# Kernel tuning notes

Hardware: AMD Instinct MI355X
Metric: run time of the kernel (lower is better)

The kernel has to match this reference:

```python
import jax, jax.numpy as jnp
import numpy as np

WS = 8
HEADS = 8


def _conv3(x, w, groups=1):
    return jax.lax.conv_general_dilated(
        x, w, (1, 1), 'SAME',
        dimension_numbers=('NCHW', 'OIHW', 'NCHW'),
        feature_group_count=groups)


def _bn(x, g, b, eps=1e-5):
    # training-mode batchnorm (batch statistics), per-channel over (B,H,W)
    m = x.mean(axis=(0, 2, 3), keepdims=True)
    v = x.var(axis=(0, 2, 3), keepdims=True)
    return (x - m) * jax.lax.rsqrt(v + eps) * g[None, :, None, None] + b[None, :, None, None]


def _relu6(x):
    return jnp.clip(x, 0.0, 6.0)


def _forward(x, w_iem, g_iem, b_iem, w_nem, g_nem, b_nem,
             w_iem_dw, w_nem_dw, w_q, w_k, w_v, w_proj, temperature):
    b, C, hp, wp = x.shape
    heads = temperature.shape[1]
    d = C // heads
    ws = WS
    nh, nw = hp // ws, wp // ws  # H,W chosen divisible by ws -> no padding

    iem_out = _relu6(_bn(_conv3(x, w_iem), g_iem, b_iem))
    illumination_map = _conv3(iem_out, w_iem_dw, groups=C)
    nem_out = _relu6(_bn(_conv3(x, w_nem), g_nem, b_nem))
    noise_map = _conv3(nem_out, w_nem_dw, groups=C)

    illum_scalar = illumination_map.mean(axis=1, keepdims=True)  # [b,1,H,W]
    noise_scalar = noise_map.mean(axis=1, keepdims=True)

    # 1x1 convs as channel matmuls
    q = jnp.einsum('oc,bchw->bohw', w_q, illumination_map)
    k = jnp.einsum('oc,bchw->bohw', w_k, noise_map)
    v = jnp.einsum('oc,bchw->bohw', w_v, x)

    def to_windows(t):  # [b,C,H,W] -> [b,heads,nh,nw,ws*ws,d]
        t = t.reshape(b, heads, d, hp, wp).transpose(0, 1, 3, 4, 2)
        t = t.reshape(b, heads, nh, ws, nw, ws, d).transpose(0, 1, 2, 4, 3, 5, 6)
        return t.reshape(b, heads, nh, nw, ws * ws, d)

    def scalar_to_windows(t):  # [b,1,H,W] -> [b,1,nh,nw,ws*ws,1]
        t = t.reshape(b, 1, nh, ws, nw, ws).transpose(0, 1, 2, 4, 3, 5)
        return t.reshape(b, 1, nh, nw, ws * ws, 1)

    qw, kw, vw = to_windows(q), to_windows(k), to_windows(v)
    illum_w = scalar_to_windows(illum_scalar)
    noise_w = scalar_to_windows(noise_scalar)

    qw = qw / jnp.maximum(jnp.linalg.norm(qw, axis=-1, keepdims=True), 1e-12)
    kw = kw / jnp.maximum(jnp.linalg.norm(kw, axis=-1, keepdims=True), 1e-12)
    qw = qw * (1.0 + illum_w)
    kw = kw * jnp.clip(1.0 - noise_w, 0.0, 1.0)

    scale = d ** (-0.5)
    attn = jnp.einsum('bhnmqd,bhnmkd->bhnmqk', qw, kw) * scale
    attn = attn * temperature  # temperature: [1,heads,1,1,1,1]
    attn = jax.nn.softmax(attn, axis=-1)
    outw = jnp.einsum('bhnmqk,bhnmkd->bhnmqd', attn, vw)

    outw = outw.reshape(b, heads, nh, nw, ws, ws, d).transpose(0, 1, 6, 2, 4, 3, 5)
    out = outw.reshape(b, C, hp, wp)
    return jnp.einsum('oc,bchw->bohw', w_proj, out)


def setup_inputs() -> dict:
    key = jax.random.key(0)
    ks = jax.random.split(key, 10)
    C = 256
    B, H, W = 2, 256, 256

    def w(k, shape):
        return jax.random.normal(k, shape, jnp.float32) * 0.05

    return {
        'x': jax.random.normal(ks[0], (B, C, H, W), jnp.float32),
        'w_iem': w(ks[1], (C, C, 3, 3)),
        'g_iem': jnp.ones((C,), jnp.float32),
        'b_iem': jnp.zeros((C,), jnp.float32),
        'w_nem': w(ks[2], (C, C, 3, 3)),
        'g_nem': jnp.ones((C,), jnp.float32),
        'b_nem': jnp.zeros((C,), jnp.float32),
        'w_iem_dw': w(ks[3], (C, 1, 3, 3)),
        'w_nem_dw': w(ks[4], (C, 1, 3, 3)),
        'w_q': w(ks[5], (C, C)),
        'w_k': w(ks[6], (C, C)),
        'w_v': w(ks[7], (C, C)),
        'w_proj': w(ks[8], (C, C)),
        'temperature': jnp.ones((1, HEADS, 1, 1, 1, 1), jnp.float32),
    }


def reference(x, w_iem, g_iem, b_iem, w_nem, g_nem, b_nem,
              w_iem_dw, w_nem_dw, w_q, w_k, w_v, w_proj, temperature):
    return _forward(x, w_iem, g_iem, b_iem, w_nem, g_nem, b_nem,
                    w_iem_dw, w_nem_dw, w_q, w_k, w_v, w_proj, temperature)
```

## Files before the change

kernel.cpp:

```cpp
#include <hip/hip_runtime.h>
#include <math.h>

constexpr int Bn  = 2;
constexpr int C   = 256;
constexpr int H   = 256;
constexpr int W   = 256;
constexpr int HW  = H * W;
constexpr size_t CHW = (size_t)C * HW;

typedef __bf16 bf16x8 __attribute__((ext_vector_type(8)));
typedef float  f32x4  __attribute__((ext_vector_type(4)));

__device__ __forceinline__ unsigned short f2bf(float f) {
    unsigned int u = __float_as_uint(f);
    u += 0x7fffu + ((u >> 16) & 1u);
    return (unsigned short)(u >> 16);
}
__device__ __forceinline__ float bf2f(unsigned short h) {
    return __uint_as_float(((unsigned int)h) << 16);
}
__device__ __forceinline__ float bflo(unsigned int u) { return __uint_as_float(u << 16); }
__device__ __forceinline__ float bfhi(unsigned int u) { return __uint_as_float(u & 0xffff0000u); }

__device__ __forceinline__ bf16x8 u2b(uint4 u) {
    union { uint4 a; bf16x8 b; } c; c.a = u; return c.b;
}

__device__ __forceinline__ void gld_lds16(const void* g, void* lds) {
    __builtin_amdgcn_global_load_lds(
        (const __attribute__((address_space(1))) unsigned int*)g,
        (__attribute__((address_space(3))) unsigned int*)lds, 16, 0, 0);
}

__device__ __forceinline__ int swz2048(int bid) {
    return ((bid & 7) << 8) | (bid >> 3);
}

__global__ __launch_bounds__(256) void packx_k(
    const float* __restrict__ x, unsigned short* __restrict__ xT)
{
    __shared__ float tl[64][65];
    const int id = blockIdx.x;
    const int ct = id & 3;
    const size_t px0 = (size_t)(id >> 2) * 64;
    const int b  = (int)(px0 >> 16);
    const int hw = (int)(px0 & 65535);
    const int c0 = ct * 64;
    const int t  = threadIdx.x;

    {
        const int cl = t >> 2, pseg = t & 3;
        const float* src = x + ((size_t)(b * C + c0 + cl)) * HW + hw + pseg * 16;
#pragma unroll
        for (int i = 0; i < 4; i++) {
            float4 v = *(const float4*)(src + i * 4);
            tl[cl][pseg * 16 + i * 4 + 0] = v.x;
            tl[cl][pseg * 16 + i * 4 + 1] = v.y;
            tl[cl][pseg * 16 + i * 4 + 2] = v.z;
            tl[cl][pseg * 16 + i * 4 + 3] = v.w;
        }
    }
    __syncthreads();
    {
        const int pl = t >> 2, csec = t & 3;
        __attribute__((aligned(16))) unsigned short rv[16];
#pragma unroll
        for (int j = 0; j < 16; j++) rv[j] = f2bf(tl[csec * 16 + j][pl]);
        unsigned short* dst = xT + (px0 + pl) * C + c0 + csec * 16;
        *(uint4*)dst       = *(const uint4*)&rv[0];
        *(uint4*)(dst + 8) = *(const uint4*)&rv[8];
    }
}

__global__ __launch_bounds__(256) void pack_k(
    const float* __restrict__ w, unsigned short* __restrict__ out, int taps)
{
    const int e = blockIdx.x * 256 + threadIdx.x;
    const int kslot = e & 31;
    const int ocl   = (e >> 5) & 127;
    const int icc   = (e >> 12) & 7;
    const int oct   = (e >> 15) & 1;
    const int off   = e >> 16;
    const int oc = oct * 128 + ocl;
    const int q  = kslot >> 3, j = kslot & 7;
    const int ic = icc * 32 + ((q ^ ((ocl >> 2) & 3)) << 3) + j;
    out[e] = f2bf(w[((size_t)oc * C + ic) * taps + off]);
}

__global__ __launch_bounds__(256) void pack4_k(
    const float* __restrict__ wq, const float* __restrict__ wk,
    const float* __restrict__ wv, const float* __restrict__ wp,
    unsigned short* __restrict__ oq, unsigned short* __restrict__ ok,
    unsigned short* __restrict__ ov, unsigned short* __restrict__ op)
{
    const int bid  = blockIdx.x;
    const int wsel = bid >> 8;
    const int e    = (bid & 255) * 256 + threadIdx.x;
    const float* w = (wsel == 0) ? wq : (wsel == 1) ? wk : (wsel == 2) ? wv : wp;
    unsigned short* out = (wsel == 0) ? oq : (wsel == 1) ? ok : (wsel == 2) ? ov : op;
    const int kslot = e & 31;
    const int ocl   = (e >> 5) & 127;
    const int icc   = (e >> 12) & 7;
    const int oct   = (e >> 15) & 1;
    const int oc = oct * 128 + ocl;
    const int q  = kslot >> 3, j = kslot & 7;
    const int ic = icc * 32 + ((q ^ ((ocl >> 2) & 3)) << 3) + j;
    out[e] = f2bf(w[(size_t)oc * C + ic]);
}

__global__ __launch_bounds__(256, 2) void conv2_k(
    const unsigned short* __restrict__ xT,
    const unsigned short* __restrict__ Wp0, const unsigned short* __restrict__ Wp1,
    unsigned short* __restrict__ out0, unsigned short* __restrict__ out1,
    const unsigned short* __restrict__ zbuf, float* __restrict__ stats_part)
{
    __shared__ unsigned short As[2][2][128 * 32];
    __shared__ unsigned short Bs[2][128 * 32];
    __shared__ float sstat[2][128][2];

    const int id  = swz2048(blockIdx.x);
    const int oct = id & 1;
    const int ch  = (id >> 1) & 1;
    const int r   = (id >> 2) & 255;
    const int b   = id >> 10;
    const int px0 = ch * 128;

    const int t  = threadIdx.x;
    const int wv = t >> 6;
    const int l  = t & 63;
    const int wm = (wv >> 1) * 64;
    const int wn = (wv & 1) * 64;

    ((float*)sstat)[t]       = 0.f;
    ((float*)sstat)[t + 256] = 0.f;

    const int qp = (l >> 4) ^ ((l >> 2) & 3);
    int a_off[4], b_off[4];
#pragma unroll
    for (int i = 0; i < 4; i++) {
        a_off[i] = (wm + i * 16 + (l & 15)) * 64 + qp * 16;
        b_off[i] = (wn + i * 16 + (l & 15)) * 64 + qp * 16;
    }
    const int spx_base = wv * 32 + (l >> 2);
    const int skk0 = (((l & 3) ^ (l >> 4)) << 3);

    const int off_lo = (r == 0) ? 3 : 0;
    const int off_hi = (r == 255) ? 6 : 9;

    f32x4 acc[2][4][4];
#pragma unroll
    for (int s = 0; s < 2; s++)
#pragma unroll
        for (int i = 0; i < 4; i++)
#pragma unroll
            for (int j = 0; j < 4; j++) acc[s][i][j] = (f32x4){0.f, 0.f, 0.f, 0.f};

#pragma unroll 1
    for (int off = off_lo; off < off_hi; ++off) {
        const int dy = off / 3, dx = off - dy * 3;
        const int rr = r + dy - 1;
        const size_t rowpix = (size_t)(b * HW) + (size_t)rr * W;
#pragma unroll 1
        for (int ip = 0; ip < 4; ++ip) {
            __syncthreads();
            const size_t wofs = ((size_t)(((off * 2 + oct) * 8 + ip * 2)) * 4096) * 2
                                + wv * 2048 + l * 16;
#pragma unroll
            for (int kc = 0; kc < 2; kc++) {
                char* A0 = (char*)As[0][kc] + wv * 2048;
                char* A1 = (char*)As[1][kc] + wv * 2048;
                const size_t o = wofs + (size_t)kc * 8192;
                gld_lds16((const char*)Wp0 + o, A0);
                gld_lds16((const char*)Wp0 + o + 1024, A0 + 1024);
                gld_lds16((const char*)Wp1 + o, A1);
                gld_lds16((const char*)Wp1 + o + 1024, A1 + 1024);
                const int ic0 = (ip * 2 + kc) * 32;
                char* BsB = (char*)Bs[kc] + wv * 2048;
#pragma unroll
                for (int i = 0; i < 2; i++) {
                    const int px = spx_base + i * 16;
                    const int cx = px0 + px + dx - 1;
                    const void* g = ((unsigned)cx > 255u)
                        ? (const void*)zbuf
                        : (const void*)(xT + ((rowpix + cx) * C + ic0 + skk0));
                    gld_lds16(g, BsB + i * 1024);
                }
            }
            asm volatile("s_waitcnt vmcnt(0)" ::: "memory");
            __syncthreads();
#pragma unroll
            for (int kc = 0; kc < 2; kc++) {
                bf16x8 af0[4], af1[4], bfr[4];
#pragma unroll
                for (int i = 0; i < 4; i++) {
                    af0[i] = *(const bf16x8*)((const char*)As[0][kc] + a_off[i]);
                    af1[i] = *(const bf16x8*)((const char*)As[1][kc] + a_off[i]);
                }
#pragma unroll
                for (int i = 0; i < 4; i++)
                    bfr[i] = *(const bf16x8*)((const char*)Bs[kc] + b_off[i]);
#pragma unroll
                for (int mi = 0; mi < 4; mi++)
#pragma unroll
                    for (int nj = 0; nj < 4; nj++) {
                        acc[0][mi][nj] = __builtin_amdgcn_mfma_f32_16x16x32_bf16(
                            af0[mi], bfr[nj], acc[0][mi][nj], 0, 0, 0);
                        acc[1][mi][nj] = __builtin_amdgcn_mfma_f32_16x16x32_bf16(
                            af1[mi], bfr[nj], acc[1][mi][nj], 0, 0, 0);
                    }
            }
        }
    }

    const int colpx = px0 + wn + (l & 15);
    const int rowoc = oct * 128 + wm + (l >> 4) * 4;
#pragma unroll
    for (int s = 0; s < 2; s++) {
        unsigned short* ob = s ? out1 : out0;
#pragma unroll
        for (int mi = 0; mi < 4; mi++) {
#pragma unroll
            for (int rg = 0; rg < 4; rg++) {
                const int oc = rowoc + mi * 16 + rg;
                float ps = 0.f, pq = 0.f;
#pragma unroll
                for (int nj = 0; nj < 4; nj++) {
                    const float v = acc[s][mi][nj][rg];
                    ps += v;
                    pq = fmaf(v, v, pq);
                    const int px = colpx + nj * 16;
                    const size_t idx = ((size_t)(b * C + oc)) * HW + (size_t)r * W + px;
                    ob[idx] = f2bf(v);
                }
                ps += __shfl_xor(ps, 1);  pq += __shfl_xor(pq, 1);
                ps += __shfl_xor(ps, 2);  pq += __shfl_xor(pq, 2);
                ps += __shfl_xor(ps, 4);  pq += __shfl_xor(pq, 4);
                ps += __shfl_xor(ps, 8);  pq += __shfl_xor(pq, 8);
                if ((l & 15) == 0) {
                    const int loc = wm + (l >> 4) * 4 + mi * 16 + rg;
                    atomicAdd(&sstat[s][loc][0], ps);
                    atomicAdd(&sstat[s][loc][1], pq);
                }
            }
        }
    }
    __syncthreads();
    stats_part[(size_t)id * 512 + t * 2 + 0] = ((float(*)[2])sstat)[t][0];
    stats_part[(size_t)id * 512 + t * 2 + 1] = ((float(*)[2])sstat)[t][1];
}

__global__ __launch_bounds__(256) void bn_reduce_k(
    const float* __restrict__ stats_part,
    const float* __restrict__ g0, const float* __restrict__ b0,
    const float* __restrict__ g1, const float* __restrict__ b1,
    float* __restrict__ scl0, float* __restrict__ shf0,
    float* __restrict__ scl1, float* __restrict__ shf1)
{
    const int s   = blockIdx.x >> 8;
    const int gc  = blockIdx.x & 255;
    const int oct = gc >> 7;
    const int loc = gc & 127;
    const int t   = threadIdx.x;
    const int ent = (s * 128 + loc) * 2;

    float ps = 0.f, pq = 0.f;
#pragma unroll
    for (int m = 0; m < 4; m++) {
        const int id = oct + 2 * (t + 256 * m);
        ps += stats_part[(size_t)id * 512 + ent];
        pq += stats_part[(size_t)id * 512 + ent + 1];
    }
    __shared__ float rs[256], rq[256];
    rs[t] = ps; rq[t] = pq;
    __syncthreads();
    for (int o = 128; o > 0; o >>= 1) {
        if (t < o) { rs[t] += rs[t + o]; rq[t] += rq[t + o]; }
        __syncthreads();
    }
    if (t == 0) {
        const float n    = (float)Bn * HW;
        const float mean = rs[0] / n;
        const float var  = rq[0] / n - mean * mean;
        const float g    = s ? g1[gc] : g0[gc];
        const float be   = s ? b1[gc] : b0[gc];
        const float sc   = g * rsqrtf(var + 1e-5f);
        if (s) { scl1[gc] = sc; shf1[gc] = be - mean * sc; }
        else   { scl0[gc] = sc; shf0[gc] = be - mean * sc; }
    }
}

__global__ __launch_bounds__(256, 2) void gemm2_k(
    const unsigned short* __restrict__ qin, const unsigned short* __restrict__ kin,
    const unsigned short* __restrict__ Wpq, const unsigned short* __restrict__ Wpk,
    unsigned short* __restrict__ outq, unsigned short* __restrict__ outk)
{
    __shared__ unsigned short As[2][2][128 * 32];
    __shared__ unsigned short Bs[2][2][128 * 32];

    const int id  = swz2048(blockIdx.x);
    const int oct = id & 1;
    const int ch  = (id >> 1) & 1;
    const int r   = (id >> 2) & 255;
    const int b   = id >> 10;
    const int px0 = ch * 128;

    const int t  = threadIdx.x;
    const int wv = t >> 6;
    const int l  = t & 63;
    const int wm = (wv >> 1) * 64;
    const int wn = (wv & 1) * 64;

    const int qp = (l >> 4) ^ ((l >> 2) & 3);
    int a_off[4], b_off[4];
#pragma unroll
    for (int i = 0; i < 4; i++) {
        a_off[i] = (wm + i * 16 + (l & 15)) * 64 + qp * 16;
        b_off[i] = (wn + i * 16 + (l & 15)) * 64 + qp * 16;
    }
    const int spx_base = wv * 32 + (l >> 2);
    const int skk0 = (((l & 3) ^ (l >> 4)) << 3);

    const size_t rowpix = (size_t)(b * HW) + (size_t)r * W;

    f32x4 acc[2][4][4];
#pragma unroll
    for (int s = 0; s < 2; s++)
#pragma unroll
        for (int i = 0; i < 4; i++)
#pragma unroll
            for (int j = 0; j < 4; j++) acc[s][i][j] = (f32x4){0.f, 0.f, 0.f, 0.f};

#pragma unroll 1
    for (int ip = 0; ip < 4; ++ip) {
        __syncthreads();
#pragma unroll
        for (int kc = 0; kc < 2; kc++) {
            const int icc = ip * 2 + kc;
            const size_t wofs = ((size_t)(oct * 8 + icc) * 4096) * 2 + wv * 2048 + l * 16;
            char* Aq = (char*)As[0][kc] + wv * 2048;
            char* Ak = (char*)As[1][kc] + wv * 2048;
            gld_lds16((const char*)Wpq + wofs, Aq);
            gld_lds16((const char*)Wpq + wofs + 1024, Aq + 1024);
            gld_lds16((const char*)Wpk + wofs, Ak);
            gld_lds16((const char*)Wpk + wofs + 1024, Ak + 1024);
            const int ic0 = icc * 32;
            char* Bq = (char*)Bs[0][kc] + wv * 2048;
            char* Bk = (char*)Bs[1][kc] + wv * 2048;
#pragma unroll
            for (int i = 0; i < 2; i++) {
                const int cx = px0 + spx_base + i * 16;
                gld_lds16((const void*)(qin + ((rowpix + cx) * C + ic0 + skk0)), Bq + i * 1024);
                gld_lds16((const void*)(kin + ((rowpix + cx) * C + ic0 + skk0)), Bk + i * 1024);
            }
        }
        asm volatile("s_waitcnt vmcnt(0)" ::: "memory");
        __syncthreads();
#pragma unroll
        for (int kc = 0; kc < 2; kc++) {
#pragma unroll
            for (int s = 0; s < 2; s++) {
                bf16x8 af[4], bfr[4];
#pragma unroll
                for (int i = 0; i < 4; i++) {
                    af[i]  = *(const bf16x8*)((const char*)As[s][kc] + a_off[i]);
                    bfr[i] = *(const bf16x8*)((const char*)Bs[s][kc] + b_off[i]);
                }
#pragma unroll
                for (int mi = 0; mi < 4; mi++)
#pragma unroll
                    for (int nj = 0; nj < 4; nj++)
                        acc[s][mi][nj] = __builtin_amdgcn_mfma_f32_16x16x32_bf16(
                            af[mi], bfr[nj], acc[s][mi][nj], 0, 0, 0);
            }
        }
    }

    const int colpx = px0 + wn + (l & 15);
    const int rowoc = oct * 128 + wm + (l >> 4) * 4;
    const size_t pxg = (size_t)(b * HW) + (size_t)r * W;
#pragma unroll
    for (int s = 0; s < 2; s++) {
        unsigned short* ob = s ? outk : outq;
#pragma unroll
        for (int mi = 0; mi < 4; mi++) {
#pragma unroll
            for (int nj = 0; nj < 4; nj++) {
                __attribute__((aligned(8))) unsigned short rv[4];
#pragma unroll
                for (int rg = 0; rg < 4; rg++) rv[rg] = f2bf(acc[s][mi][nj][rg]);
                const int oc = rowoc + mi * 16;
                const int px = colpx + nj * 16;
                *(uint2*)(ob + (pxg + px) * C + oc) = *(const uint2*)rv;
            }
        }
    }
}

template<bool F32OUT, bool NHWC_OUT>
__global__ __launch_bounds__(256, 4) void gemm_k(
    const unsigned short* __restrict__ xT, const unsigned short* __restrict__ Wp,
    unsigned short* __restrict__ outb, float* __restrict__ outf)
{
    __shared__ unsigned short As[2][128 * 32];
    __shared__ unsigned short Bs[2][128 * 32];

    const int id  = swz2048(blockIdx.x);
    const int oct = id & 1;
    const int ch  = (id >> 1) & 1;
    const int r   = (id >> 2) & 255;
    const int b   = id >> 10;
    const int px0 = ch * 128;

    const int t  = threadIdx.x;
    const int wv = t >> 6;
    const int l  = t & 63;
    const int wm = (wv >> 1) * 64;
    const int wn = (wv & 1) * 64;

    const int qp = (l >> 4) ^ ((l >> 2) & 3);
    int a_off[4], b_off[4];
#pragma unroll
    for (int i = 0; i < 4; i++) {
        a_off[i] = (wm + i * 16 + (l & 15)) * 64 + qp * 16;
        b_off[i] = (wn + i * 16 + (l & 15)) * 64 + qp * 16;
    }
    const int spx_base = wv * 32 + (l >> 2);
    const int skk0 = (((l & 3) ^ (l >> 4)) << 3);

    const size_t rowpix = (size_t)(b * HW) + (size_t)r * W;

    f32x4 acc[4][4];
#pragma unroll
    for (int i = 0; i < 4; i++)
#pragma unroll
        for (int j = 0; j < 4; j++) acc[i][j] = (f32x4){0.f, 0.f, 0.f, 0.f};

#pragma unroll 1
    for (int ip = 0; ip < 4; ++ip) {
        __syncthreads();
#pragma unroll
        for (int kc = 0; kc < 2; kc++) {
            const int icc = ip * 2 + kc;
            const char* Ag = (const char*)Wp +
                ((size_t)(oct * 8 + icc) * 4096) * 2 + wv * 2048 + l * 16;
            char* AsB = (char*)As[kc] + wv * 2048;
            gld_lds16(Ag, AsB);
            gld_lds16(Ag + 1024, AsB + 1024);
            const int ic0 = icc * 32;
            char* BsB = (char*)Bs[kc] + wv * 2048;
#pragma unroll
            for (int i = 0; i < 2; i++) {
                const int cx = px0 + spx_base + i * 16;
                gld_lds16((const void*)(xT + ((rowpix + cx) * C + ic0 + skk0)), BsB + i * 1024);
            }
        }
        asm volatile("s_waitcnt vmcnt(0)" ::: "memory");
        __syncthreads();
#pragma unroll
        for (int kc = 0; kc < 2; kc++) {
            bf16x8 af[4], bfr[4];
#pragma unroll
            for (int i = 0; i < 4; i++) {
                af[i]  = *(const bf16x8*)((const char*)As[kc] + a_off[i]);
                bfr[i] = *(const bf16x8*)((const char*)Bs[kc] + b_off[i]);
            }
#pragma unroll
            for (int mi = 0; mi < 4; mi++)
#pragma unroll
                for (int nj = 0; nj < 4; nj++)
                    acc[mi][nj] = __builtin_amdgcn_mfma_f32_16x16x32_bf16(
                        af[mi], bfr[nj], acc[mi][nj], 0, 0, 0);
        }
    }

    const int colpx = px0 + wn + (l & 15);
    const int rowoc = oct * 128 + wm + (l >> 4) * 4;
    if (NHWC_OUT) {
        const size_t pxg = (size_t)(b * HW) + (size_t)r * W;
#pragma unroll
        for (int mi = 0; mi < 4; mi++) {
#pragma unroll
            for (int nj = 0; nj < 4; nj++) {
                __attribute__((aligned(8))) unsigned short rv[4];
#pragma unroll
                for (int rg = 0; rg < 4; rg++) rv[rg] = f2bf(acc[mi][nj][rg]);
                const int oc = rowoc + mi * 16;
                const int px = colpx + nj * 16;
                *(uint2*)(outb + (pxg + px) * C + oc) = *(const uint2*)rv;
            }
        }
    } else {
#pragma unroll
        for (int mi = 0; mi < 4; mi++) {
#pragma unroll
            for (int nj = 0; nj < 4; nj++) {
#pragma unroll
                for (int rg = 0; rg < 4; rg++) {
                    const int oc = rowoc + mi * 16 + rg;
                    const int px = colpx + nj * 16;
                    const size_t idx = ((size_t)(b * C + oc)) * HW + (size_t)r * W + px;
                    if (F32OUT) outf[idx] = acc[mi][nj][rg];
                    else        outb[idx] = f2bf(acc[mi][nj][rg]);
                }
            }
        }
    }
}

__global__ __launch_bounds__(256) void dwconv_k(
    const unsigned short* __restrict__ a0, const unsigned short* __restrict__ a1,
    const float* __restrict__ scl0, const float* __restrict__ shf0,
    const float* __restrict__ scl1, const float* __restrict__ shf1,
    const float* __restrict__ wd0, const float* __restrict__ wd1,
    unsigned short* __restrict__ out0, unsigned short* __restrict__ out1,
    float* __restrict__ sm0, float* __restrict__ sm1)
{
    __shared__ float tile[32][3][67];
    __shared__ float wds[32 * 9];
    __shared__ float sscl[32], sshf[32];

    const int id  = blockIdx.x;
    const int c0  = (id & 7) * 32;
    const int w0  = ((id >> 3) & 3) * 64;
    const int r   = (id >> 5) & 255;
    const int b   = (id >> 13) & 1;
    const int set = id >> 14;
    const int t   = threadIdx.x;

    const unsigned short* a   = set ? a1 : a0;
    const float* scale        = set ? scl1 : scl0;
    const float* shift        = set ? shf1 : shf0;
    const float* wd           = set ? wd1 : wd0;
    unsigned short* out       = set ? out1 : out0;
    float* smean              = set ? sm1 : sm0;

    for (int i = t; i < 288; i += 256) wds[i] = wd[c0 * 9 + i];
    if (t < 32) { sscl[t] = scale[c0 + t]; sshf[t] = shift[c0 + t]; }
    __syncthreads();

    for (int i = t; i < 1536; i += 256) {
        const int c   = i / 48;
        const int rem = i - c * 48;
        const int row = rem >> 4, seg = rem & 15;
        const int rr  = r + row - 1;
        float f0 = 0.f, f1 = 0.f, f2 = 0.f, f3 = 0.f;
        if ((unsigned)rr < 256u) {
            const uint2 v = *(const uint2*)(a + ((size_t)(b * C + c0 + c)) * HW
                                              + (size_t)rr * W + w0 + seg * 4);
            const float sc = sscl[c], sh = sshf[c];
            f0 = fminf(fmaxf(fmaf(bflo(v.x), sc, sh), 0.f), 6.f);
            f1 = fminf(fmaxf(fmaf(bfhi(v.x), sc, sh), 0.f), 6.f);
            f2 = fminf(fmaxf(fmaf(bflo(v.y), sc, sh), 0.f), 6.f);
            f3 = fminf(fmaxf(fmaf(bfhi(v.y), sc, sh), 0.f), 6.f);
        }
        float* dst = &tile[c][row][1 + seg * 4];
        dst[0] = f0; dst[1] = f1; dst[2] = f2; dst[3] = f3;
    }
    for (int i = t; i < 192; i += 256) {
        const int c   = i / 6;
        const int rem = i - c * 6;
        const int row = rem >> 1, side = rem & 1;
        const int rr  = r + row - 1;
        const int col = side ? (w0 + 64) : (w0 - 1);
        float v = 0.f;
        if ((unsigned)rr < 256u && (unsigned)col < 256u) {
            float u = bf2f(a[((size_t)(b * C + c0 + c)) * HW + (size_t)rr * W + col]);
            v = fminf(fmaxf(fmaf(u, sscl[c], sshf[c]), 0.f), 6.f);
        }
        tile[c][row][side ? 65 : 0] = v;
    }
    __syncthreads();

    const int px = t >> 2, csub = t & 3;
    __attribute__((aligned(16))) unsigned short res[8];
    float psum = 0.f;
#pragma unroll
    for (int k = 0; k < 8; k++) {
        const int c = csub * 8 + k;
        const float* wp = &wds[c * 9];
        float accv = 0.f;
#pragma unroll
        for (int dy = 0; dy < 3; dy++)
#pragma unroll
            for (int dx = 0; dx < 3; dx++)
                accv = fmaf(tile[c][dy][px + dx], wp[dy * 3 + dx], accv);
        res[k] = f2bf(accv);
        psum += accv;
    }
    unsigned short* o = out + ((size_t)(b * HW) + (size_t)r * W + w0 + px) * C + c0 + csub * 8;
    *(uint4*)o = *(const uint4*)&res[0];

    psum += __shfl_xor(psum, 1);
    psum += __shfl_xor(psum, 2);
    if (csub == 0)
        atomicAdd(&smean[(size_t)(b * HW) + (size_t)r * W + w0 + px], psum * (1.f / C));
}

__global__ __launch_bounds__(64) void attn_k(
    const unsigned short* __restrict__ q, const unsigned short* __restrict__ k,
    const unsigned short* __restrict__ v, const float* __restrict__ si,
    const float* __restrict__ sn, const float* __restrict__ temp,
    unsigned short* __restrict__ out)
{
    __shared__ unsigned short Pl[64][72];
    __shared__ unsigned short Vt[32][72];

    const int id   = blockIdx.x;
    const int wx   = id & 31;
    const int wy   = (id >> 5) & 31;
    const int head = (id >> 10) & 7;
    const int b    = id >> 13;
    const int l    = threadIdx.x;
    const int pl15 = l & 15;
    const int g    = l >> 4;
    const int ch0  = head * 32;
    const int base = wy * 8 * W + wx * 8;
    const size_t bb = (size_t)b * HW;

    uint4 qv[4], kv[4];
    float qss[4], kss[4];
#pragma unroll
    for (int i = 0; i < 4; i++) {
        const int p = i * 16 + pl15;
        const size_t a = (bb + base + (p >> 3) * W + (p & 7)) * C + ch0 + g * 8;
        qv[i] = *(const uint4*)(q + a);
        kv[i] = *(const uint4*)(k + a);
        float s0 = 0.f, s1 = 0.f;
        {
            uint4 u = qv[i];
            float f;
            f = bflo(u.x); s0 = fmaf(f, f, s0);  f = bfhi(u.x); s0 = fmaf(f, f, s0);
            f = bflo(u.y); s0 = fmaf(f, f, s0);  f = bfhi(u.y); s0 = fmaf(f, f, s0);
            f = bflo(u.z); s0 = fmaf(f, f, s0);  f = bfhi(u.z); s0 = fmaf(f, f, s0);
            f = bflo(u.w); s0 = fmaf(f, f, s0);  f = bfhi(u.w); s0 = fmaf(f, f, s0);
        }
        {
            uint4 u = kv[i];
            float f;
            f = bflo(u.x); s1 = fmaf(f, f, s1);  f = bfhi(u.x); s1 = fmaf(f, f, s1);
            f = bflo(u.y); s1 = fmaf(f, f, s1);  f = bfhi(u.y); s1 = fmaf(f, f, s1);
            f = bflo(u.z); s1 = fmaf(f, f, s1);  f = bfhi(u.z); s1 = fmaf(f, f, s1);
            f = bflo(u.w); s1 = fmaf(f, f, s1);  f = bfhi(u.w); s1 = fmaf(f, f, s1);
        }
        s0 += __shfl_xor(s0, 16); s0 += __shfl_xor(s0, 32);
        s1 += __shfl_xor(s1, 16); s1 += __shfl_xor(s1, 32);
        qss[i] = s0; kss[i] = s1;
    }

    {
        const size_t a = (bb + base + (l >> 3) * W + (l & 7)) * C + ch0;
        const uint4* vp = (const uint4*)(v + a);
#pragma unroll
        for (int i = 0; i < 4; i++) {
            uint4 vv = vp[i];
            Vt[i * 8 + 0][l] = (unsigned short)(vv.x);
            Vt[i * 8 + 1][l] = (unsigned short)(vv.x >> 16);
            Vt[i * 8 + 2][l] = (unsigned short)(vv.y);
            Vt[i * 8 + 3][l] = (unsigned short)(vv.y >> 16);
            Vt[i * 8 + 4][l] = (unsigned short)(vv.z);
            Vt[i * 8 + 5][l] = (unsigned short)(vv.z >> 16);
            Vt[i * 8 + 6][l] = (unsigned short)(vv.w);
            Vt[i * 8 + 7][l] = (unsigned short)(vv.w >> 16);
        }
    }

    const float tsc = temp[head] * 0.17677669529663689f;
    float qmul[4], kscl[4];
#pragma unroll
    for (int i = 0; i < 4; i++) {
        const int p = i * 16 + pl15;
        const size_t pg = bb + base + (p >> 3) * W + (p & 7);
        const float il = si[pg];
        const float nz = sn[pg];
        qmul[i] = (1.f + il) * tsc / fmaxf(sqrtf(qss[i]), 1e-12f);
        kscl[i] = fminf(fmaxf(1.f - nz, 0.f), 1.f) / fmaxf(sqrtf(kss[i]), 1e-12f);
    }

    f32x4 acc[4][4];
    __builtin_amdgcn_s_setprio(1);
#pragma unroll
    for (int qi = 0; qi < 4; qi++)
#pragma unroll
        for (int kj = 0; kj < 4; kj++)
            acc[qi][kj] = __builtin_amdgcn_mfma_f32_16x16x32_bf16(
                u2b(qv[qi]), u2b(kv[kj]), (f32x4){0.f, 0.f, 0.f, 0.f}, 0, 0, 0);
    __builtin_amdgcn_s_setprio(0);

    float inv[4][4];
#pragma unroll
    for (int qi = 0; qi < 4; qi++) {
#pragma unroll
        for (int rg = 0; rg < 4; rg++) {
            const float qm = __shfl(qmul[qi], (g << 2) + rg);
            float s[4];
#pragma unroll
            for (int kj = 0; kj < 4; kj++) s[kj] = acc[qi][kj][rg] * kscl[kj] * qm;
            float mx = fmaxf(fmaxf(s[0], s[1]), fmaxf(s[2], s[3]));
            mx = fmaxf(mx, __shfl_xor(mx, 1));
            mx = fmaxf(mx, __shfl_xor(mx, 2));
            mx = fmaxf(mx, __shfl_xor(mx, 4));
            mx = fmaxf(mx, __shfl_xor(mx, 8));
            float sum = 0.f;
#pragma unroll
            for (int kj = 0; kj < 4; kj++) {
                const float e = __expf(s[kj] - mx);
                acc[qi][kj][rg] = e;
                sum += e;
            }
            sum += __shfl_xor(sum, 1);
            sum += __shfl_xor(sum, 2);
            sum += __shfl_xor(sum, 4);
            sum += __shfl_xor(sum, 8);
            inv[qi][rg] = 1.f / sum;
            const int qrow = qi * 16 + (g << 2) + rg;
#pragma unroll
            for (int kj = 0; kj < 4; kj++)
                Pl[qrow][pl15 + 16 * kj] = f2bf(acc[qi][kj][rg]);
        }
    }

    f32x4 oacc[4][2];
#pragma unroll
    for (int qi = 0; qi < 4; qi++)
#pragma unroll
        for (int dj = 0; dj < 2; dj++) oacc[qi][dj] = (f32x4){0.f, 0.f, 0.f, 0.f};

#pragma unroll
    for (int kc = 0; kc < 2; kc++) {
        const bf16x8 vb0 = *(const bf16x8*)&Vt[pl15][kc * 32 + g * 8];
        const bf16x8 vb1 = *(const bf16x8*)&Vt[pl15 + 16][kc * 32 + g * 8];
        __builtin_amdgcn_s_setprio(1);
#pragma unroll
        for (int qi = 0; qi < 4; qi++) {
            const bf16x8 pa = *(const bf16x8*)&Pl[qi * 16 + pl15][kc * 32 + g * 8];
            oacc[qi][0] = __builtin_amdgcn_mfma_f32_16x16x32_bf16(pa, vb0, oacc[qi][0], 0, 0, 0);
            oacc[qi][1] = __builtin_amdgcn_mfma_f32_16x16x32_bf16(pa, vb1, oacc[qi][1], 0, 0, 0);
        }
        __builtin_amdgcn_s_setprio(0);
    }

#pragma unroll
    for (int qi = 0; qi < 4; qi++) {
#pragma unroll
        for (int rg = 0; rg < 4; rg++) {
            const int qrow = qi * 16 + (g << 2) + rg;
            const size_t oaddr = (bb + base + (qrow >> 3) * W + (qrow & 7)) * C + ch0;
            const float sc = inv[qi][rg];
            out[oaddr + pl15]      = f2bf(oacc[qi][0][rg] * sc);
            out[oaddr + 16 + pl15] = f2bf(oacc[qi][1][rg] * sc);
        }
    }
}

extern "C" void kernel_launch(void* const* d_in, const int* in_sizes, int n_in,
                              void* d_out, int out_size, void* d_ws, size_t ws_size,
                              hipStream_t stream)
{
    const float* x        = (const float*)d_in[0];
    const float* w_iem    = (const float*)d_in[1];
    const float* g_iem    = (const float*)d_in[2];
    const float* b_iem    = (const float*)d_in[3];
    const float* w_nem    = (const float*)d_in[4];
    const float* g_nem    = (const float*)d_in[5];
    const float* b_nem    = (const float*)d_in[6];
    const float* w_iem_dw = (const float*)d_in[7];
    const float* w_nem_dw = (const float*)d_in[8];
    const float* w_q      = (const float*)d_in[9];
    const float* w_k      = (const float*)d_in[10];
    const float* w_v      = (const float*)d_in[11];
    const float* w_proj   = (const float*)d_in[12];
    const float* temp     = (const float*)d_in[13];

    char* p = (char*)d_ws;
    unsigned short* zbuf = (unsigned short*)p;      p += 256;
    float* scl0 = (float*)p;                        p += 256 * 4;
    float* shf0 = (float*)p;                        p += 256 * 4;
    float* scl1 = (float*)p;                        p += 256 * 4;
    float* shf1 = (float*)p;                        p += 256 * 4;
    float* stats_part = (float*)p;                  p += (size_t)2048 * 512 * 4;
    float* sI  = (float*)p;                         p += (size_t)Bn * HW * 4;
    float* sN  = (float*)p;                         p += (size_t)Bn * HW * 4;
    unsigned short* Wp_iem = (unsigned short*)p;    p += 589824 * 2;
    unsigned short* Wp_nem = (unsigned short*)p;    p += 589824 * 2;
    unsigned short* Wpq = (unsigned short*)p;       p += 65536 * 2;
    unsigned short* Wpk = (unsigned short*)p;       p += 65536 * 2;
    unsigned short* Wpv = (unsigned short*)p;       p += 65536 * 2;
    unsigned short* Wpp = (unsigned short*)p;       p += 65536 * 2;
    unsigned short* xT   = (unsigned short*)p;      p += Bn * CHW * 2;
    unsigned short* bufA = (unsigned short*)p;      p += Bn * CHW * 2;
    unsigned short* Ibf  = (unsigned short*)p;      p += Bn * CHW * 2;
    unsigned short* Nbf  = (unsigned short*)p;      p += Bn * CHW * 2;
    unsigned short* Obf  = (unsigned short*)p;      p += Bn * CHW * 2;

    hipMemsetAsync(zbuf, 0, 256, stream);
    hipMemsetAsync(sI, 0, (size_t)Bn * HW * 4 * 2, stream);

    packx_k<<<8192, 256, 0, stream>>>(x, xT);
    pack_k<<<2304, 256, 0, stream>>>(w_iem, Wp_iem, 9);
    pack_k<<<2304, 256, 0, stream>>>(w_nem, Wp_nem, 9);
    pack4_k<<<1024, 256, 0, stream>>>(w_q, w_k, w_v, w_proj, Wpq, Wpk, Wpv, Wpp);

    conv2_k<<<2048, 256, 0, stream>>>(xT, Wp_iem, Wp_nem, bufA, Obf, zbuf, stats_part);
    bn_reduce_k<<<512, 256, 0, stream>>>(stats_part, g_iem, b_iem, g_nem, b_nem,
                                         scl0, shf0, scl1, shf1);

    dwconv_k<<<32768, 256, 0, stream>>>(bufA, Obf, scl0, shf0, scl1, shf1,
                                        w_iem_dw, w_nem_dw, Ibf, Nbf, sI, sN);

    gemm2_k<<<2048, 256, 0, stream>>>(Ibf, Nbf, Wpq, Wpk, bufA, Obf);
    gemm_k<false, true><<<2048, 256, 0, stream>>>(xT, Wpv, Nbf, nullptr);

    attn_k<<<16384, 64, 0, stream>>>(bufA, Obf, Nbf, sI, sN, temp, Ibf);

    gemm_k<true, false><<<2048, 256, 0, stream>>>(Ibf, Wpp, nullptr, (float*)d_out);
}
```

Measured before the change: 1.014 ms.

## Share one haloed input row tile across all three horizontal conv taps

Restructures the implicit-GEMM 3x3 conv loop so that, for each vertical tap and 32-channel chunk, a single 130-pixel haloed input row is loaded into LDS once. The three horizontal taps then read shifted slices of it, while the weights for all three dx taps are staged at the same time. This cuts redundant global loads of the activation tile from three per row to one, and it has fewer sync barriers per unit of MFMA work. In exchange, LDS use rises (three weight buffers), the swizzle addressing becomes more complex, and a few threads handle the halo load.

```diff
diff --git a/kernel.cpp b/kernel.cpp
--- a/kernel.cpp
+++ b/kernel.cpp
@@ -114,8 +114,8 @@
     unsigned short* __restrict__ out0, unsigned short* __restrict__ out1,
     const unsigned short* __restrict__ zbuf, float* __restrict__ stats_part)
 {
-    __shared__ unsigned short As[2][2][128 * 32];
-    __shared__ unsigned short Bs[2][128 * 32];
+    __shared__ unsigned short As[3][2][128 * 32];
+    __shared__ unsigned short Bs[136 * 32];
     __shared__ float sstat[2][128][2];
 
     const int id  = swz2048(blockIdx.x);
@@ -130,22 +130,19 @@
     const int l  = t & 63;
     const int wm = (wv >> 1) * 64;
     const int wn = (wv & 1) * 64;
+    const int g  = l >> 4;
 
     ((float*)sstat)[t]       = 0.f;
     ((float*)sstat)[t + 256] = 0.f;
 
     const int qp = (l >> 4) ^ ((l >> 2) & 3);
-    int a_off[4], b_off[4];
-#pragma unroll
-    for (int i = 0; i < 4; i++) {
+    int a_off[4];
+#pragma unroll
+    for (int i = 0; i < 4; i++)
         a_off[i] = (wm + i * 16 + (l & 15)) * 64 + qp * 16;
-        b_off[i] = (wn + i * 16 + (l & 15)) * 64 + qp * 16;
-    }
-    const int spx_base = wv * 32 + (l >> 2);
-    const int skk0 = (((l & 3) ^ (l >> 4)) << 3);
-
-    const int off_lo = (r == 0) ? 3 : 0;
-    const int off_hi = (r == 255) ? 6 : 9;
+
+    const int dy_lo = (r == 0) ? 1 : 0;
+    const int dy_hi = (r == 255) ? 1 : 2;
 
     f32x4 acc[2][4][4];
 #pragma unroll
@@ -156,49 +153,61 @@
             for (int j = 0; j < 4; j++) acc[s][i][j] = (f32x4){0.f, 0.f, 0.f, 0.f};
 
 #pragma unroll 1
-    for (int off = off_lo; off < off_hi; ++off) {
-        const int dy = off / 3, dx = off - dy * 3;
+    for (int dy = dy_lo; dy <= dy_hi; ++dy) {
         const int rr = r + dy - 1;
         const size_t rowpix = (size_t)(b * HW) + (size_t)rr * W;
 #pragma unroll 1
-        for (int ip = 0; ip < 4; ++ip) {
+        for (int icc = 0; icc < 8; ++icc) {
             __syncthreads();
-            const size_t wofs = ((size_t)(((off * 2 + oct) * 8 + ip * 2)) * 4096) * 2
-                                + wv * 2048 + l * 16;
-#pragma unroll
-            for (int kc = 0; kc < 2; kc++) {
-                char* A0 = (char*)As[0][kc] + wv * 2048;
-                char* A1 = (char*)As[1][kc] + wv * 2048;
-                const size_t o = wofs + (size_t)kc * 8192;
-                gld_lds16((const char*)Wp0 + o, A0);
-                gld_lds16((const char*)Wp0 + o + 1024, A0 + 1024);
-                gld_lds16((const char*)Wp1 + o, A1);
-                gld_lds16((const char*)Wp1 + o + 1024, A1 + 1024);
-                const int ic0 = (ip * 2 + kc) * 32;
-                char* BsB = (char*)Bs[kc] + wv * 2048;
-#pragma unroll
-                for (int i = 0; i < 2; i++) {
-                    const int px = spx_base + i * 16;
-                    const int cx = px0 + px + dx - 1;
-                    const void* g = ((unsigned)cx > 255u)
-                        ? (const void*)zbuf
-                        : (const void*)(xT + ((rowpix + cx) * C + ic0 + skk0));
-                    gld_lds16(g, BsB + i * 1024);
-                }
+#pragma unroll
+            for (int dxt = 0; dxt < 3; dxt++) {
+                const int off = dy * 3 + dxt;
+                const size_t wofs = ((size_t)(((off * 2 + oct) * 8 + icc)) * 4096) * 2
+                                    + wv * 2048 + l * 16;
+                char* A0 = (char*)As[dxt][0] + wv * 2048;
+                char* A1 = (char*)As[dxt][1] + wv * 2048;
+                gld_lds16((const char*)Wp0 + wofs, A0);
+                gld_lds16((const char*)Wp0 + wofs + 1024, A0 + 1024);
+                gld_lds16((const char*)Wp1 + wofs, A1);
+                gld_lds16((const char*)Wp1 + wofs + 1024, A1 + 1024);
+            }
+            const int ic0 = icc * 32;
+#pragma unroll
+            for (int i = 0; i < 2; i++) {
+                const int j   = wv * 16 + (l >> 2) + i * 64;
+                const int gpx = px0 + j - 1;
+                const int kg  = (l & 3) ^ ((j >> 2) & 3);
+                const void* gsrc = ((unsigned)gpx > 255u)
+                    ? (const void*)zbuf
+                    : (const void*)(xT + ((rowpix + gpx) * C + ic0 + kg * 8));
+                gld_lds16(gsrc, (char*)Bs + wv * 1024 + i * 4096);
+            }
+            if (t < 8) {
+                const int j   = 128 + (l >> 2);
+                const int gpx = px0 + j - 1;
+                const int kg  = (l & 3) ^ ((j >> 2) & 3);
+                const void* gsrc = ((unsigned)gpx > 255u)
+                    ? (const void*)zbuf
+                    : (const void*)(xT + ((rowpix + gpx) * C + ic0 + kg * 8));
+                gld_lds16(gsrc, (char*)Bs + 8192);
             }
             asm volatile("s_waitcnt vmcnt(0)" ::: "memory");
             __syncthreads();
 #pragma unroll
-            for (int kc = 0; kc < 2; kc++) {
-                bf16x8 af0[4], af1[4], bfr[4];
+            for (int dxt = 0; dxt < 3; dxt++) {
+                bf16x8 bfr[4];
 #pragma unroll
                 for (int i = 0; i < 4; i++) {
-                    af0[i] = *(const bf16x8*)((const char*)As[0][kc] + a_off[i]);
-                    af1[i] = *(const bf16x8*)((const char*)As[1][kc] + a_off[i]);
+                    const int j  = wn + i * 16 + (l & 15) + dxt;
+                    const int bq = g ^ ((j >> 2) & 3);
+                    bfr[i] = *(const bf16x8*)((const char*)Bs + j * 64 + bq * 16);
                 }
-#pragma unroll
-                for (int i = 0; i < 4; i++)
-                    bfr[i] = *(const bf16x8*)((const char*)Bs[kc] + b_off[i]);
+                bf16x8 af0[4], af1[4];
+#pragma unroll
+                for (int i = 0; i < 4; i++) {
+                    af0[i] = *(const bf16x8*)((const char*)As[dxt][0] + a_off[i]);
+                    af1[i] = *(const bf16x8*)((const char*)As[dxt][1] + a_off[i]);
+                }
 #pragma unroll
                 for (int mi = 0; mi < 4; mi++)
 #pragma unroll
```

Result: faster. 992.7 us (-2.1%).
